# Optimization experiments

Hardware: AMD Instinct MI355X
Metric: run time of the kernel (lower is better)

Reference implementation:

```python
import jax, jax.numpy as jnp
import numpy as np

B, T, D, H, W = 4, 2048, 256, 512, 32
EPS = 1e-5


def _xavier(key, fan_in, fan_out):
    # torch xavier_uniform on weight [out, in]; stored here as [in, out]
    limit = float(np.sqrt(6.0 / (fan_in + fan_out)))
    return jax.random.uniform(key, (fan_in, fan_out), jnp.float32, -limit, limit)


def _bias(key, fan_in, fan_out):
    # torch Linear default bias init: U(-1/sqrt(fan_in), 1/sqrt(fan_in))
    limit = float(1.0 / np.sqrt(fan_in))
    return jax.random.uniform(key, (fan_out,), jnp.float32, -limit, limit)


def setup_inputs() -> dict:
    key = jax.random.key(0)
    ks = jax.random.split(key, 16)
    inp = {
        "feature": jax.random.normal(ks[0], (B, T, D), jnp.float32),
        "gamma": jnp.ones((D,), jnp.float32),
        "beta": jnp.zeros((D,), jnp.float32),
        "w1": _xavier(ks[1], D, H), "b1": _bias(ks[2], D, H),
        "w2": _xavier(ks[3], H, H), "b2": _bias(ks[4], H, H),
        "w3": _xavier(ks[5], D, H), "b3": _bias(ks[6], H, H),
        "w4": _xavier(ks[7], H, H), "b4": _bias(ks[8], H, H),
        "w5": _xavier(ks[9], D, H), "b5": _bias(ks[10], H, H),
        "w6": _xavier(ks[11], H, H), "b6": _bias(ks[12], H, H),
        "window": W,
    }
    return inp


def reference(feature, gamma, beta, w1, b1, w2, b2, w3, b3, w4, b4, w5, b5, w6, b6, window):
    Bsz, Tlen, Din = feature.shape
    nb = Tlen // window
    x = feature.reshape(Bsz, nb, window, Din)  # [B, nb, W, D] window blocks

    # LayerNorm over last dim
    mu = jnp.mean(x, axis=-1, keepdims=True)
    var = jnp.mean((x - mu) ** 2, axis=-1, keepdims=True)
    n = (x - mu) * jax.lax.rsqrt(var + EPS) * gamma + beta

    Q = jnp.tanh(n @ w1 + b1) @ w2 + b2  # [B, nb, W, H]
    K = jnp.tanh(n @ w3 + b3) @ w4 + b4
    V = jax.nn.relu(n @ w5 + b5) @ w6 + b6

    Hdim = w2.shape[1]
    sqrt_feat = jnp.sqrt(jnp.float32(Hdim))
    sqrt_time = jnp.sqrt(jnp.float32(window))

    # time-axis attention: [B, nb, W, W]
    beta_time = jnp.einsum('bnwh,bnvh->bnwv', Q, K) / sqrt_feat
    # feature-axis attention: [B, nb, H, H]
    beta_feat = jnp.einsum('bnwh,bnwg->bnhg', Q, K) / sqrt_time

    A_time = jax.nn.softmax(beta_time, axis=-1)
    A_feat = jax.nn.softmax(beta_feat, axis=-2)

    feat = jnp.einsum('bnwh,bnhg->bnwg', V, A_feat)   # V @ A_feat
    out = jnp.einsum('bnwv,bnvg->bnwg', A_time, feat)  # A_time @ (V @ A_feat)
    return out.reshape(Bsz, Tlen, Hdim)
```

## Files before the change

### kernel.cpp

```cpp
#include <hip/hip_runtime.h>
#include <hip/hip_bf16.h>

typedef unsigned short u16;
typedef __attribute__((ext_vector_type(8))) unsigned short ushort8;
typedef __attribute__((ext_vector_type(8))) short short8;
typedef __attribute__((ext_vector_type(4))) float f32x4;
typedef __attribute__((ext_vector_type(4))) unsigned uint4_t;

#define DEV __device__ __forceinline__

DEV float b2f(u16 u){ return __uint_as_float(((unsigned)u) << 16); }
DEV unsigned cvtpk(float lo, float hi){
  unsigned r;
  asm("v_cvt_pk_bf16_f32 %0, %1, %2" : "=v"(r) : "v"(lo), "v"(hi));
  return r;
}
DEV u16 f2b(float f){ return (u16)cvtpk(f, f); }
DEV void pl32swap(unsigned& a, unsigned& b){
  asm("v_permlane32_swap_b32 %0, %1" : "+v"(a), "+v"(b));
}
DEV void pl16swap(unsigned& a, unsigned& b){
  asm("v_permlane16_swap_b32 %0, %1" : "+v"(a), "+v"(b));
}
DEV float fexp2(float x){
  float r;
  asm("v_exp_f32 %0, %1" : "=v"(r) : "v"(x));
  return r;
}
DEV float frcp(float x){
  float r;
  asm("v_rcp_f32 %0, %1" : "=v"(r) : "v"(x));
  return r;
}
DEV short8 ld8(const u16* p){ return __builtin_bit_cast(short8, *(const ushort8*)p); }
DEV f32x4 mfma(short8 a, short8 b, f32x4 c){
  return __builtin_amdgcn_mfma_f32_16x16x32_bf16(a, b, c, 0, 0, 0);
}
DEV float fast_tanh(float x){
  float e = fexp2(x * 2.8853900817779268f);
  return 1.f - 2.f * frcp(e + 1.f);
}
DEV unsigned pk2(float lo, float hi){ return cvtpk(lo, hi); }

__global__ __launch_bounds__(256) void prep_k(
    const float* __restrict__ w1, const float* __restrict__ w2,
    const float* __restrict__ w3, const float* __restrict__ w4,
    const float* __restrict__ w5, const float* __restrict__ w6,
    u16* __restrict__ ws,
    const float* __restrict__ xg, const float* __restrict__ gg,
    const float* __restrict__ bgm, u16* __restrict__ ng)
{
  __shared__ u16 tile[64][72];
  const int bid = blockIdx.x;
  if (bid < 384) {
    const int z = bid / 64, rem = bid % 64, by = rem / 8, bx = rem % 8;
    const float* w; u16* wt; int K;
    switch (z) {
      case 0:  w = w1; wt = ws;          K = 256; break;
      case 1:  w = w2; wt = ws + 131072; K = 512; break;
      case 2:  w = w3; wt = ws + 393216; K = 256; break;
      case 3:  w = w4; wt = ws + 524288; K = 512; break;
      case 4:  w = w5; wt = ws + 786432; K = 256; break;
      default: w = w6; wt = ws + 917504; K = 512; break;
    }
    int k0 = by * 64;
    if (k0 >= K) return;
    int n0 = bx * 64;
    int t = threadIdx.x;
    int r = t >> 2, c0 = (t & 3) * 16;
    const float* src = w + (size_t)(k0 + r) * 512 + n0 + c0;
    #pragma unroll
    for (int jj = 0; jj < 4; ++jj) {
      float4 v = *(const float4*)(src + jj * 4);
      unsigned* tp = (unsigned*)&tile[r][c0 + jj*4];
      tp[0] = cvtpk(v.x, v.y);
      tp[1] = cvtpk(v.z, v.w);
    }
    __syncthreads();
    ushort8 o0, o1;
    #pragma unroll
    for (int j = 0; j < 8; ++j) { o0[j] = tile[c0 + j][r]; o1[j] = tile[c0 + 8 + j][r]; }
    u16* dst = wt + (size_t)(n0 + r) * K + k0 + c0;
    *(ushort8*)dst       = o0;
    *(ushort8*)(dst + 8) = o1;
  } else {
    const int lb = bid - 384;
    int row = lb * 8 + (threadIdx.x >> 5);
    int l32 = threadIdx.x & 31;
    const float* xr = xg + (size_t)row*256 + l32*8;
    float xf[8];
    #pragma unroll
    for (int j = 0; j < 8; j += 4) {
      float4 v = *(const float4*)(xr + j);
      xf[j] = v.x; xf[j+1] = v.y; xf[j+2] = v.z; xf[j+3] = v.w;
    }
    float s = 0.f, ss = 0.f;
    #pragma unroll
    for (int j = 0; j < 8; ++j){ s += xf[j]; ss += xf[j]*xf[j]; }
    #pragma unroll
    for (int m = 1; m < 32; m <<= 1){ s += __shfl_xor(s, m); ss += __shfl_xor(ss, m); }
    float mean = s * (1.f/256.f);
    float var  = ss * (1.f/256.f) - mean*mean;
    float rs   = rsqrtf(var + 1e-5f);
    float r8[8];
    #pragma unroll
    for (int j = 0; j < 8; j += 4) {
      float4 gv = *(const float4*)(gg  + l32*8 + j);
      float4 bv = *(const float4*)(bgm + l32*8 + j);
      r8[j]   = (xf[j]   - mean)*rs*gv.x + bv.x;
      r8[j+1] = (xf[j+1] - mean)*rs*gv.y + bv.y;
      r8[j+2] = (xf[j+2] - mean)*rs*gv.z + bv.z;
      r8[j+3] = (xf[j+3] - mean)*rs*gv.w + bv.w;
    }
    uint4_t o;
    o[0] = cvtpk(r8[0], r8[1]); o[1] = cvtpk(r8[2], r8[3]);
    o[2] = cvtpk(r8[4], r8[5]); o[3] = cvtpk(r8[6], r8[7]);
    *(uint4_t*)(ng + (size_t)row*256 + l32*8) = o;
  }
}

template<int NS, int ACT>
__global__ __launch_bounds__(512, 4) void gemm_tile(
    const u16* __restrict__ Abase, size_t a_zstride,
    const u16* __restrict__ wst, int w_off0,
    const float* __restrict__ bz0, const float* __restrict__ bz1, const float* __restrict__ bz2,
    u16* __restrict__ Cbase)
{
  constexpr int KA = NS * 32;
  __shared__ __align__(16) u16 sm[20480];
  u16* smA = sm;
  u16* smB = sm + 10240;
  const int z = blockIdx.z;
  const u16* A = Abase + (size_t)z * a_zstride;
  const u16* W = wst + w_off0 + z * 393216;
  const float* bias = (z == 0) ? bz0 : ((z == 1) ? bz1 : bz2);
  u16* C = Cbase + (size_t)z * 4194304;
  const int M0 = blockIdx.x * 128, N0 = blockIdx.y * 128;
  const int tid = threadIdx.x;
  const int wv = tid >> 6, ln = tid & 63, q = ln >> 4, r16 = ln & 15;
  const int m0w = (wv >> 2) * 64, n0w = (wv & 3) * 32;
  const f32x4 Z = {0.f, 0.f, 0.f, 0.f};

  const int srow = tid >> 2, scq = (tid & 3) * 8;
  const u16* gA = A + (size_t)(M0 + srow) * KA + scq;
  const u16* gB = W + (size_t)(N0 + srow) * KA + scq;
  u16* dA = smA + srow * 40 + scq;
  u16* dB = smB + srow * 40 + scq;

  ushort8 rA[2], rB[2];
  rA[0] = *(const ushort8*)gA;
  rB[0] = *(const ushort8*)gB;
  *(ushort8*)dA = rA[0];
  *(ushort8*)dB = rB[0];
  if (NS > 1) { rA[1] = *(const ushort8*)(gA + 32); rB[1] = *(const ushort8*)(gB + 32); }
  __syncthreads();

  f32x4 acc[4][2];
  #pragma unroll
  for (int mf = 0; mf < 4; ++mf){ acc[mf][0] = Z; acc[mf][1] = Z; }

  #pragma unroll
  for (int kk = 0; kk < NS; ++kk) {
    const int cur = kk & 1;
    const u16* bufA = smA + cur * 5120;
    const u16* bufB = smB + cur * 5120;
    short8 aF[4], bF[2];
    #pragma unroll
    for (int mf = 0; mf < 4; ++mf) aF[mf] = ld8(bufA + (m0w + mf*16 + r16)*40 + q*8);
    #pragma unroll
    for (int nf = 0; nf < 2; ++nf) bF[nf] = ld8(bufB + (n0w + nf*16 + r16)*40 + q*8);
    #pragma unroll
    for (int mf = 0; mf < 4; ++mf)
      #pragma unroll
      for (int nf = 0; nf < 2; ++nf)
        acc[mf][nf] = mfma(aF[mf], bF[nf], acc[mf][nf]);
    if (kk + 1 < NS) {
      *(ushort8*)(dA + (cur ^ 1) * 5120) = rA[(kk + 1) & 1];
      *(ushort8*)(dB + (cur ^ 1) * 5120) = rB[(kk + 1) & 1];
    }
    if (kk + 2 < NS) {
      rA[kk & 1] = *(const ushort8*)(gA + (kk + 2) * 32);
      rB[kk & 1] = *(const ushort8*)(gB + (kk + 2) * 32);
    }
    __syncthreads();
  }

  u16* ct = sm;
  #pragma unroll
  for (int nf = 0; nf < 2; ++nf) {
    int colL = n0w + nf*16 + r16;
    float bs = bias[N0 + colL];
    #pragma unroll
    for (int mf = 0; mf < 4; ++mf)
      #pragma unroll
      for (int i = 0; i < 4; ++i) {
        int row = m0w + mf*16 + q*4 + i;
        float v = acc[mf][nf][i] + bs;
        if (ACT == 1) v = fmaxf(v, 0.f);
        else if (ACT == 3) v = (z == 2) ? fmaxf(v, 0.f) : fast_tanh(v);
        ct[row*132 + colL] = f2b(v);
      }
  }
  __syncthreads();
  #pragma unroll
  for (int j = 0; j < 4; ++j) {
    int row = (tid >> 4) + j*32;
    int cb2 = (tid & 15) * 8;
    ushort8 vv = *(const ushort8*)(ct + row*132 + cb2);
    *(ushort8*)(C + (size_t)(M0 + row)*512 + N0 + cb2) = vv;
  }
}

#define AV   0
#define AQT  16640
#define AKT  37120
#define ABT  57600
#define AAT  59712
#define ASM_ELS 60992

__global__ __launch_bounds__(1024) void attn_k(
    const u16* __restrict__ QKVg, float* __restrict__ outg)
{
  __shared__ __align__(16) u16 sm[ASM_ELS];
  const int tid = threadIdx.x;
  const int bid = blockIdx.x;
  const int wv = tid >> 6, ln = tid & 63, q = ln >> 4, r16 = ln & 15;
  const f32x4 Z = {0.f, 0.f, 0.f, 0.f};
  const float RS512 = 0.04419417382415922f;
  const float C32L2 = 0.25500526676986233f;
  const float LOG2E = 1.4426950408889634f;
  const u16* Qg = QKVg + (size_t)bid * 16384;
  const u16* Kg = QKVg + 4194304 + (size_t)bid * 16384;
  const u16* Vg = QKVg + 8388608 + (size_t)bid * 16384;

  float* btf = (float*)(sm + ABT);
  if (wv < 4) {
    int mt = wv >> 1, nt = wv & 1;
    f32x4 acc = Z;
    const u16* qb = Qg + (mt*16 + r16)*512;
    const u16* kb = Kg + (nt*16 + r16)*512;
    #pragma unroll
    for (int kk = 0; kk < 16; ++kk)
      acc = mfma(ld8(qb + kk*32 + q*8), ld8(kb + kk*32 + q*8), acc);
    #pragma unroll
    for (int i = 0; i < 4; ++i)
      btf[(mt*16 + q*4 + i)*33 + nt*16 + r16] = acc[i] * RS512;
  } else if (wv < 12) {
    int t1 = tid - 256;
    int rp = t1 & 15;
    int cb = (t1 >> 4) * 16;
    const u16* s0 = Qg + (2*rp)*512 + cb;
    const u16* s1 = s0 + 512;
    ushort8 a0 = *(const ushort8*)s0, a1 = *(const ushort8*)(s0 + 8);
    ushort8 c0v = *(const ushort8*)s1, c1v = *(const ushort8*)(s1 + 8);
    unsigned* qt32 = (unsigned*)(sm + AQT);
    #pragma unroll
    for (int j = 0; j < 8; ++j) {
      qt32[(cb + j)*20 + rp]     = (unsigned)a0[j] | ((unsigned)c0v[j] << 16);
      qt32[(cb + 8 + j)*20 + rp] = (unsigned)a1[j] | ((unsigned)c1v[j] << 16);
    }
  } else {
    int t2 = tid - 768;
    int vrow = t2 >> 3, seg = (t2 & 7) * 64;
    const u16* src = Vg + vrow*512 + seg;
    #pragma unroll
    for (int jj = 0; jj < 8; ++jj)
      *(ushort8*)(sm + AV + vrow*520 + seg + jj*8) = *(const ushort8*)(src + jj*8);
  }
  __syncthreads();

  if (tid < 512) {
    int row = tid >> 4, v2 = tid & 15;
    float v0 = btf[row*33 + v2], v1 = btf[row*33 + v2 + 16];
    float m = fmaxf(v0, v1);
    #pragma unroll
    for (int msk = 1; msk < 16; msk <<= 1) m = fmaxf(m, __shfl_xor(m, msk));
    float e0 = fexp2((v0 - m) * LOG2E), e1 = fexp2((v1 - m) * LOG2E);
    float sum = e0 + e1;
    #pragma unroll
    for (int msk = 1; msk < 16; msk <<= 1) sum += __shfl_xor(sum, msk);
    float inv = frcp(sum);
    sm[AAT + row*40 + v2]      = f2b(e0 * inv);
    sm[AAT + row*40 + v2 + 16] = f2b(e1 * inv);
  } else {
    int t1 = tid - 512;
    int rp = t1 & 15;
    int cb = (t1 >> 4) * 16;
    const u16* s0 = Kg + (2*rp)*512 + cb;
    const u16* s1 = s0 + 512;
    ushort8 a0 = *(const ushort8*)s0, a1 = *(const ushort8*)(s0 + 8);
    ushort8 c0v = *(const ushort8*)s1, c1v = *(const ushort8*)(s1 + 8);
    unsigned* kt32 = (unsigned*)(sm + AKT);
    #pragma unroll
    for (int j = 0; j < 8; ++j) {
      kt32[(cb + j)*20 + rp]     = (unsigned)a0[j] | ((unsigned)c0v[j] << 16);
      kt32[(cb + 8 + j)*20 + rp] = (unsigned)a1[j] | ((unsigned)c1v[j] << 16);
    }
  }
  __syncthreads();

  {
    const int g0 = wv * 32;
    f32x4 facc[2][2];
    facc[0][0]=Z; facc[0][1]=Z; facc[1][0]=Z; facc[1][1]=Z;
    float csum[2] = {0.f, 0.f};
    short8 bK[2];
    #pragma unroll
    for (int gt = 0; gt < 2; ++gt)
      bK[gt] = ld8(sm + AKT + (size_t)(g0 + gt*16 + r16)*40 + q*8);

    short8 aQn0 = ld8(sm + AQT + (r16)*40 + q*8);
    short8 aQn1 = ld8(sm + AQT + (16 + r16)*40 + q*8);

    #pragma unroll 2
    for (int ht = 0; ht < 16; ++ht) {
      short8 aQ0 = aQn0, aQ1 = aQn1;
      if (ht < 15) {
        aQn0 = ld8(sm + AQT + ((ht+1)*32 + r16)*40 + q*8);
        aQn1 = ld8(sm + AQT + ((ht+1)*32 + 16 + r16)*40 + q*8);
      }
      f32x4 sv[2][2];
      #pragma unroll
      for (int gt = 0; gt < 2; ++gt) {
        sv[0][gt] = mfma(aQ0, bK[gt], Z);
        sv[1][gt] = mfma(aQ1, bK[gt], Z);
      }
      unsigned D[2][4];
      #pragma unroll
      for (int gt = 0; gt < 2; ++gt) {
        float e[2][4];
        #pragma unroll
        for (int smi = 0; smi < 2; ++smi)
          #pragma unroll
          for (int i = 0; i < 4; ++i) {
            float ev = fexp2(sv[smi][gt][i] * C32L2);
            e[smi][i] = ev;
            csum[gt] += ev;
          }
        #pragma unroll
        for (int k = 0; k < 2; ++k) {
          unsigned w0 = cvtpk(e[0][2*k], e[0][2*k+1]);
          unsigned w1 = cvtpk(e[1][2*k], e[1][2*k+1]);
          pl32swap(w0, w1);
          pl16swap(w0, w1);
          D[gt][k]     = w0;
          D[gt][k + 2] = w1;
        }
      }
      #pragma unroll
      for (int mt = 0; mt < 2; ++mt) {
        short8 aV = ld8(sm + AV + (mt*16 + r16)*520 + ht*32 + q*8);
        #pragma unroll
        for (int gt = 0; gt < 2; ++gt) {
          uint4_t dv = {D[gt][0], D[gt][1], D[gt][2], D[gt][3]};
          short8 bE = __builtin_bit_cast(short8, dv);
          facc[mt][gt] = mfma(aV, bE, facc[mt][gt]);
        }
      }
    }
    float inv[2];
    #pragma unroll
    for (int gt = 0; gt < 2; ++gt) {
      float cs = csum[gt];
      cs += __shfl_xor(cs, 16);
      cs += __shfl_xor(cs, 32);
      inv[gt] = frcp(cs);
    }
    unsigned F[2][4];
    #pragma unroll
    for (int gt = 0; gt < 2; ++gt) {
      float e0n[4], e1n[4];
      #pragma unroll
      for (int i = 0; i < 4; ++i) {
        e0n[i] = facc[0][gt][i] * inv[gt];
        e1n[i] = facc[1][gt][i] * inv[gt];
      }
      #pragma unroll
      for (int k = 0; k < 2; ++k) {
        unsigned w0 = cvtpk(e0n[2*k], e0n[2*k+1]);
        unsigned w1 = cvtpk(e1n[2*k], e1n[2*k+1]);
        pl32swap(w0, w1);
        pl16swap(w0, w1);
        F[gt][k]     = w0;
        F[gt][k + 2] = w1;
      }
    }
    short8 aA0 = ld8(sm + AAT + r16*40 + q*8);
    short8 aA1 = ld8(sm + AAT + (16 + r16)*40 + q*8);
    #pragma unroll
    for (int gt = 0; gt < 2; ++gt) {
      uint4_t fv = {F[gt][0], F[gt][1], F[gt][2], F[gt][3]};
      short8 bF = __builtin_bit_cast(short8, fv);
      f32x4 o0 = mfma(aA0, bF, Z);
      f32x4 o1 = mfma(aA1, bF, Z);
      #pragma unroll
      for (int i = 0; i < 4; ++i) {
        int g = g0 + gt*16 + r16;
        outg[(size_t)(bid*32 + q*4 + i)*512 + g]      = o0[i];
        outg[(size_t)(bid*32 + 16 + q*4 + i)*512 + g] = o1[i];
      }
    }
  }
}


#define OFF_V   0
#define OFF_N   16640
#define OFF_T   25088
#define OFF_Q   41728
#define OFF_K   58368
#define OFF_BT  75008
#define OFF_QT  16640
#define OFF_KT  37120
#define OFF_AT  78080
#define OFF_FT  37120
#define SMEM_ELS 79360

template<int ACT>
DEV void mlp_branch(const u16* __restrict__ nl, u16* __restrict__ tl, u16* __restrict__ ol,
                    const u16* __restrict__ wA, const float* __restrict__ bA,
                    const u16* __restrict__ wB, const float* __restrict__ bB,
                    int wv, int q, int r16)
{
  const f32x4 Z = {0.f, 0.f, 0.f, 0.f};
  const int c0 = wv*32 + r16;
  float biasA0 = bA[c0], biasA1 = bA[c0 + 16];
  float biasB0 = bB[c0], biasB1 = bB[c0 + 16];
  {
    const u16* cp0 = wA + (size_t)c0*256 + q*8;
    const u16* cp1 = cp0 + 16*256;
    const u16* a0p = nl + r16 * 264 + q*8;
    const u16* a1p = nl + (16 + r16) * 264 + q*8;
    f32x4 acc[2][2];
    acc[0][0]=Z; acc[0][1]=Z; acc[1][0]=Z; acc[1][1]=Z;
    #pragma unroll
    for (int kk = 0; kk < 8; ++kk) {
      short8 a0 = ld8(a0p + kk*32);
      short8 a1 = ld8(a1p + kk*32);
      short8 b0 = ld8(cp0 + kk*32);
      short8 b1 = ld8(cp1 + kk*32);
      acc[0][0] = mfma(a0, b0, acc[0][0]);
      acc[1][0] = mfma(a1, b0, acc[1][0]);
      acc[0][1] = mfma(a0, b1, acc[0][1]);
      acc[1][1] = mfma(a1, b1, acc[1][1]);
    }
    #pragma unroll
    for (int gt = 0; gt < 2; ++gt) {
      float bias = gt ? biasA1 : biasA0;
      #pragma unroll
      for (int mt = 0; mt < 2; ++mt)
        #pragma unroll
        for (int i = 0; i < 4; ++i) {
          float v = acc[mt][gt][i] + bias;
          v = (ACT == 0) ? fast_tanh(v) : fmaxf(v, 0.f);
          tl[(mt*16 + q*4 + i)*520 + c0 + gt*16] = f2b(v);
        }
    }
  }
  __syncthreads();
  {
    const u16* cp0 = wB + (size_t)c0*512 + q*8;
    const u16* cp1 = cp0 + 16*512;
    const u16* a0p = tl + r16 * 520 + q*8;
    const u16* a1p = tl + (16 + r16) * 520 + q*8;
    f32x4 acc[2][2];
    acc[0][0]=Z; acc[0][1]=Z; acc[1][0]=Z; acc[1][1]=Z;
    #pragma unroll
    for (int kk = 0; kk < 16; ++kk) {
      short8 a0 = ld8(a0p + kk*32);
      short8 a1 = ld8(a1p + kk*32);
      short8 b0 = ld8(cp0 + kk*32);
      short8 b1 = ld8(cp1 + kk*32);
      acc[0][0] = mfma(a0, b0, acc[0][0]);
      acc[1][0] = mfma(a1, b0, acc[1][0]);
      acc[0][1] = mfma(a0, b1, acc[0][1]);
      acc[1][1] = mfma(a1, b1, acc[1][1]);
    }
    #pragma unroll
    for (int gt = 0; gt < 2; ++gt) {
      float bias = gt ? biasB1 : biasB0;
      #pragma unroll
      for (int mt = 0; mt < 2; ++mt)
        #pragma unroll
        for (int i = 0; i < 4; ++i)
          ol[(mt*16 + q*4 + i)*520 + c0 + gt*16] = f2b(acc[mt][gt][i] + bias);
    }
  }
}

__global__ __launch_bounds__(1024) void fused_main(
    const float* __restrict__ xg, const float* __restrict__ gg, const float* __restrict__ bgm,
    const float* __restrict__ b1, const float* __restrict__ b2, const float* __restrict__ b3,
    const float* __restrict__ b4, const float* __restrict__ b5, const float* __restrict__ b6,
    const u16* __restrict__ wst, float* __restrict__ outg)
{
  __shared__ __align__(16) u16 sm[SMEM_ELS];
  const int tid = threadIdx.x;
  const int bid = blockIdx.x;
  const int wv = tid >> 6, ln = tid & 63, q = ln >> 4, r16 = ln & 15;
  const f32x4 Z = {0.f, 0.f, 0.f, 0.f};
  const float RS512 = 0.04419417382415922f;
  const float C32L2 = 0.25500526676986233f;

  {
    int row = tid >> 5, l32 = tid & 31;
    const float* xr = xg + (size_t)(bid*32 + row)*256 + l32*8;
    float xf[8];
    #pragma unroll
    for (int j = 0; j < 8; j += 4) {
      float4 v = *(const float4*)(xr + j);
      xf[j] = v.x; xf[j+1] = v.y; xf[j+2] = v.z; xf[j+3] = v.w;
    }
    float s = 0.f, ss = 0.f;
    #pragma unroll
    for (int j = 0; j < 8; ++j){ s += xf[j]; ss += xf[j]*xf[j]; }
    #pragma unroll
    for (int m = 1; m < 32; m <<= 1){ s += __shfl_xor(s, m); ss += __shfl_xor(ss, m); }
    float mean = s * (1.f/256.f);
    float var  = ss * (1.f/256.f) - mean*mean;
    float rs   = rsqrtf(var + 1e-5f);
    float gf[8], bf[8];
    #pragma unroll
    for (int j = 0; j < 8; j += 4) {
      float4 gv = *(const float4*)(gg  + l32*8 + j);
      float4 bv = *(const float4*)(bgm + l32*8 + j);
      gf[j] = gv.x; gf[j+1] = gv.y; gf[j+2] = gv.z; gf[j+3] = gv.w;
      bf[j] = bv.x; bf[j+1] = bv.y; bf[j+2] = bv.z; bf[j+3] = bv.w;
    }
    ushort8 o0;
    #pragma unroll
    for (int j = 0; j < 8; ++j)
      o0[j] = f2b((xf[j] - mean)*rs*gf[j] + bf[j]);
    *(ushort8*)(sm + OFF_N + row*264 + l32*8) = o0;
  }
  __syncthreads();

  mlp_branch<0>(sm+OFF_N, sm+OFF_T, sm+OFF_Q, wst,          b1, wst + 131072, b2, wv, q, r16);
  __syncthreads();
  mlp_branch<0>(sm+OFF_N, sm+OFF_T, sm+OFF_K, wst + 393216, b3, wst + 524288, b4, wv, q, r16);
  __syncthreads();
  mlp_branch<1>(sm+OFF_N, sm+OFF_T, sm+OFF_V, wst + 786432, b5, wst + 917504, b6, wv, q, r16);
  __syncthreads();

  float* btf = (float*)(sm + OFF_BT);
  if (wv < 4) {
    int mt = wv >> 1, nt = wv & 1;
    f32x4 acc = Z;
    const u16* qb = sm + OFF_Q + (mt*16 + r16)*520;
    const u16* kb = sm + OFF_K + (nt*16 + r16)*520;
    for (int kk = 0; kk < 16; ++kk)
      acc = mfma(ld8(qb + kk*32 + q*8), ld8(kb + kk*32 + q*8), acc);
    #pragma unroll
    for (int i = 0; i < 4; ++i)
      btf[(mt*16 + q*4 + i)*33 + nt*16 + r16] = acc[i] * RS512;
  } else if (wv < 12) {
    int t1 = tid - 256;
    int row = t1 & 31, cb = (t1 >> 5) * 32;
    const u16* src = sm + OFF_Q + row*520 + cb;
    ushort8 v[4];
    #pragma unroll
    for (int jj = 0; jj < 4; ++jj) v[jj] = *(const ushort8*)(src + jj*8);
    #pragma unroll
    for (int jj = 0; jj < 4; ++jj)
      #pragma unroll
      for (int j = 0; j < 8; ++j)
        sm[OFF_QT + (cb + jj*8 + j)*40 + row] = v[jj][j];
  }
  __syncthreads();

  if (tid < 512) {
    int row = tid >> 4, v2 = tid & 15;
    float v0 = btf[row*33 + v2], v1 = btf[row*33 + v2 + 16];
    float m = fmaxf(v0, v1);
    #pragma unroll
    for (int msk = 1; msk < 16; msk <<= 1) m = fmaxf(m, __shfl_xor(m, msk));
    float e0 = __expf(v0 - m), e1 = __expf(v1 - m);
    float sum = e0 + e1;
    #pragma unroll
    for (int msk = 1; msk < 16; msk <<= 1) sum += __shfl_xor(sum, msk);
    float inv = 1.f / sum;
    sm[OFF_AT + row*40 + v2]      = f2b(e0 * inv);
    sm[OFF_AT + row*40 + v2 + 16] = f2b(e1 * inv);
  } else {
    int t2 = tid - 512;
    int row = t2 & 31, cb = (t2 >> 5) * 32;
    const u16* src = sm + OFF_K + row*520 + cb;
    ushort8 v[4];
    #pragma unroll
    for (int jj = 0; jj < 4; ++jj) v[jj] = *(const ushort8*)(src + jj*8);
    #pragma unroll
    for (int jj = 0; jj < 4; ++jj)
      #pragma unroll
      for (int j = 0; j < 8; ++j)
        sm[OFF_KT + (cb + jj*8 + j)*40 + row] = v[jj][j];
  }
  __syncthreads();

  {
    const int g0 = wv * 32;
    const bool hi32 = (ln >= 32);
    const bool qodd = (q & 1);
    f32x4 facc[2][2];
    facc[0][0]=Z; facc[0][1]=Z; facc[1][0]=Z; facc[1][1]=Z;
    float csum[2] = {0.f, 0.f};
    short8 bK[2];
    #pragma unroll
    for (int gt = 0; gt < 2; ++gt)
      bK[gt] = ld8(sm + OFF_KT + (size_t)(g0 + gt*16 + r16)*40 + q*8);

    #pragma unroll 2
    for (int ht = 0; ht < 16; ++ht) {
      f32x4 sv[2][2];
      #pragma unroll
      for (int smi = 0; smi < 2; ++smi) {
        short8 aQ = ld8(sm + OFF_QT + (ht*32 + smi*16 + r16)*40 + q*8);
        #pragma unroll
        for (int gt = 0; gt < 2; ++gt)
          sv[smi][gt] = mfma(aQ, bK[gt], Z);
      }
      unsigned D[2][4];
      #pragma unroll
      for (int gt = 0; gt < 2; ++gt) {
        float e[2][4];
        #pragma unroll
        for (int smi = 0; smi < 2; ++smi)
          #pragma unroll
          for (int i = 0; i < 4; ++i) {
            float ev = fexp2(sv[smi][gt][i] * C32L2);
            e[smi][i] = ev;
            csum[gt] += ev;
          }
        #pragma unroll
        for (int k = 0; k < 2; ++k) {
          unsigned w0 = pk2(e[0][2*k], e[0][2*k+1]);
          unsigned w1 = pk2(e[1][2*k], e[1][2*k+1]);
          unsigned Pw0 = (unsigned)__shfl_xor((int)w0, 32);
          unsigned Pw1 = (unsigned)__shfl_xor((int)w1, 32);
          unsigned x = hi32 ? Pw1 : w0;
          unsigned y = hi32 ? w1 : Pw0;
          unsigned xs = (unsigned)__shfl_xor((int)x, 16);
          unsigned ys = (unsigned)__shfl_xor((int)y, 16);
          D[gt][k]     = qodd ? ys : x;
          D[gt][k + 2] = qodd ? y  : xs;
        }
      }
      #pragma unroll
      for (int mt = 0; mt < 2; ++mt) {
        short8 aV = ld8(sm + OFF_V + (mt*16 + r16)*520 + ht*32 + q*8);
        #pragma unroll
        for (int gt = 0; gt < 2; ++gt) {
          uint4_t dv = {D[gt][0], D[gt][1], D[gt][2], D[gt][3]};
          short8 bE = __builtin_bit_cast(short8, dv);
          facc[mt][gt] = mfma(aV, bE, facc[mt][gt]);
        }
      }
    }
    float inv[2];
    #pragma unroll
    for (int gt = 0; gt < 2; ++gt) {
      float cs = csum[gt];
      cs += __shfl_xor(cs, 16);
      cs += __shfl_xor(cs, 32);
      inv[gt] = 1.f / cs;
    }
    #pragma unroll
    for (int mt = 0; mt < 2; ++mt)
      #pragma unroll
      for (int gt = 0; gt < 2; ++gt)
        #pragma unroll
        for (int i = 0; i < 4; ++i) {
          int w = mt*16 + q*4 + i;
          int g = g0 + gt*16 + r16;
          sm[OFF_FT + g*40 + w] = f2b(facc[mt][gt][i] * inv[gt]);
        }
  }

  {
    const int g0 = wv * 32;
    short8 aA0 = ld8(sm + OFF_AT + r16*40 + q*8);
    short8 aA1 = ld8(sm + OFF_AT + (16 + r16)*40 + q*8);
    #pragma unroll
    for (int gt = 0; gt < 2; ++gt) {
      short8 bF = ld8(sm + OFF_FT + (size_t)(g0 + gt*16 + r16)*40 + q*8);
      f32x4 o0 = mfma(aA0, bF, Z);
      f32x4 o1 = mfma(aA1, bF, Z);
      #pragma unroll
      for (int i = 0; i < 4; ++i) {
        int g = g0 + gt*16 + r16;
        outg[(size_t)(bid*32 + q*4 + i)*512 + g]      = o0[i];
        outg[(size_t)(bid*32 + 16 + q*4 + i)*512 + g] = o1[i];
      }
    }
  }
}


extern "C" void kernel_launch(void* const* d_in, const int* in_sizes, int n_in,
                              void* d_out, int out_size, void* d_ws, size_t ws_size,
                              hipStream_t stream)
{
  const float* x  = (const float*)d_in[0];
  const float* gm = (const float*)d_in[1];
  const float* bt = (const float*)d_in[2];
  const float* w1 = (const float*)d_in[3];
  const float* b1 = (const float*)d_in[4];
  const float* w2 = (const float*)d_in[5];
  const float* b2 = (const float*)d_in[6];
  const float* w3 = (const float*)d_in[7];
  const float* b3 = (const float*)d_in[8];
  const float* w4 = (const float*)d_in[9];
  const float* b4 = (const float*)d_in[10];
  const float* w5 = (const float*)d_in[11];
  const float* b5 = (const float*)d_in[12];
  const float* w6 = (const float*)d_in[13];
  const float* b6 = (const float*)d_in[14];
  u16* ws  = (u16*)d_ws;
  float* out = (float*)d_out;

  const size_t WT_OFF  = 0;
  const size_t N_OFF   = 1179648;
  const size_t T_OFF   = 3276800;
  const size_t QKV_OFF = 15859712;
  const size_t NEED_BYTES = 28442624ULL * 2ULL;

  if (ws_size >= NEED_BYTES) {
    prep_k<<<1408, 256, 0, stream>>>(w1, w2, w3, w4, w5, w6, ws + WT_OFF,
                                     x, gm, bt, ws + N_OFF);
    gemm_tile<8, 3><<<dim3(64, 4, 3), 512, 0, stream>>>(
        ws + N_OFF, 0, ws + WT_OFF, 0, b1, b3, b5, ws + T_OFF);
    gemm_tile<16, 2><<<dim3(64, 4, 3), 512, 0, stream>>>(
        ws + T_OFF, 4194304, ws + WT_OFF, 131072, b2, b4, b6, ws + QKV_OFF);
    attn_k<<<256, 1024, 0, stream>>>(ws + QKV_OFF, out);
  } else {
    prep_k<<<384, 256, 0, stream>>>(w1, w2, w3, w4, w5, w6, ws + WT_OFF,
                                    x, gm, bt, ws + WT_OFF );
    fused_main<<<256, 1024, 0, stream>>>(x, gm, bt, b1, b2, b3, b4, b5, b6, ws + WT_OFF, out);
  }
}
```

Measured before the change: 71.48 us.

## Fuse the two MLP GEMM layers into one kernel keeping the hidden tile in LDS

Replaces the two separate tiled GEMM launches (first layer with activation, then second layer) with a single kernel. Each block computes a 64-row slice of the first-layer output across all 512 hidden columns, keeps the activated bf16 tile in shared memory, and then runs the second GEMM against it. This removes the global write and reread of the intermediate tensor and one kernel launch. In exchange, operands are loaded directly from global memory with no LDS staging or double buffering, output stores are scattered 2-byte writes, and the larger LDS footprint lowers occupancy.

Result: slower. 102.7 us (+43.7%).

```diff
diff --git a/kernel.cpp b/kernel.cpp
--- a/kernel.cpp
+++ b/kernel.cpp
@@ -119,95 +119,96 @@
   }
 }
 
-template<int NS, int ACT>
-__global__ __launch_bounds__(512, 4) void gemm_tile(
-    const u16* __restrict__ Abase, size_t a_zstride,
-    const u16* __restrict__ wst, int w_off0,
-    const float* __restrict__ bz0, const float* __restrict__ bz1, const float* __restrict__ bz2,
-    u16* __restrict__ Cbase)
+#define TSTR 516
+__global__ __launch_bounds__(512, 2) void mlp_k(
+    const u16* __restrict__ ng, const u16* __restrict__ wst,
+    const float* __restrict__ b1, const float* __restrict__ b3, const float* __restrict__ b5,
+    const float* __restrict__ b2, const float* __restrict__ b4, const float* __restrict__ b6,
+    u16* __restrict__ QKVg)
 {
-  constexpr int KA = NS * 32;
-  __shared__ __align__(16) u16 sm[20480];
-  u16* smA = sm;
-  u16* smB = sm + 10240;
-  const int z = blockIdx.z;
-  const u16* A = Abase + (size_t)z * a_zstride;
-  const u16* W = wst + w_off0 + z * 393216;
-  const float* bias = (z == 0) ? bz0 : ((z == 1) ? bz1 : bz2);
-  u16* C = Cbase + (size_t)z * 4194304;
-  const int M0 = blockIdx.x * 128, N0 = blockIdx.y * 128;
+  __shared__ __align__(16) u16 tl[64 * TSTR];
+  const int M0 = blockIdx.x * 64;
+  const int z  = blockIdx.y;
+  const u16* W1 = wst + (size_t)z * 393216;
+  const u16* W2 = wst + 131072 + (size_t)z * 393216;
+  const float* bA = (z == 0) ? b1 : ((z == 1) ? b3 : b5);
+  const float* bB = (z == 0) ? b2 : ((z == 1) ? b4 : b6);
+  u16* C = QKVg + (size_t)z * 4194304;
   const int tid = threadIdx.x;
   const int wv = tid >> 6, ln = tid & 63, q = ln >> 4, r16 = ln & 15;
-  const int m0w = (wv >> 2) * 64, n0w = (wv & 3) * 32;
   const f32x4 Z = {0.f, 0.f, 0.f, 0.f};
-
-  const int srow = tid >> 2, scq = (tid & 3) * 8;
-  const u16* gA = A + (size_t)(M0 + srow) * KA + scq;
-  const u16* gB = W + (size_t)(N0 + srow) * KA + scq;
-  u16* dA = smA + srow * 40 + scq;
-  u16* dB = smB + srow * 40 + scq;
-
-  ushort8 rA[2], rB[2];
-  rA[0] = *(const ushort8*)gA;
-  rB[0] = *(const ushort8*)gB;
-  *(ushort8*)dA = rA[0];
-  *(ushort8*)dB = rB[0];
-  if (NS > 1) { rA[1] = *(const ushort8*)(gA + 32); rB[1] = *(const ushort8*)(gB + 32); }
-  __syncthreads();
-
-  f32x4 acc[4][2];
-  #pragma unroll
-  for (int mf = 0; mf < 4; ++mf){ acc[mf][0] = Z; acc[mf][1] = Z; }
-
-  #pragma unroll
-  for (int kk = 0; kk < NS; ++kk) {
-    const int cur = kk & 1;
-    const u16* bufA = smA + cur * 5120;
-    const u16* bufB = smB + cur * 5120;
-    short8 aF[4], bF[2];
-    #pragma unroll
-    for (int mf = 0; mf < 4; ++mf) aF[mf] = ld8(bufA + (m0w + mf*16 + r16)*40 + q*8);
-    #pragma unroll
-    for (int nf = 0; nf < 2; ++nf) bF[nf] = ld8(bufB + (n0w + nf*16 + r16)*40 + q*8);
+  const u16* nA = ng + (size_t)M0 * 256;
+
+  {
+    f32x4 acc[4][4];
     #pragma unroll
     for (int mf = 0; mf < 4; ++mf)
       #pragma unroll
-      for (int nf = 0; nf < 2; ++nf)
-        acc[mf][nf] = mfma(aF[mf], bF[nf], acc[mf][nf]);
-    if (kk + 1 < NS) {
-      *(ushort8*)(dA + (cur ^ 1) * 5120) = rA[(kk + 1) & 1];
-      *(ushort8*)(dB + (cur ^ 1) * 5120) = rB[(kk + 1) & 1];
-    }
-    if (kk + 2 < NS) {
-      rA[kk & 1] = *(const ushort8*)(gA + (kk + 2) * 32);
-      rB[kk & 1] = *(const ushort8*)(gB + (kk + 2) * 32);
-    }
-    __syncthreads();
-  }
-
-  u16* ct = sm;
-  #pragma unroll
-  for (int nf = 0; nf < 2; ++nf) {
-    int colL = n0w + nf*16 + r16;
-    float bs = bias[N0 + colL];
+      for (int nf = 0; nf < 4; ++nf) acc[mf][nf] = Z;
+    #pragma unroll
+    for (int kk = 0; kk < 8; ++kk) {
+      short8 aF[4], bF[4];
+      #pragma unroll
+      for (int mf = 0; mf < 4; ++mf)
+        aF[mf] = ld8(nA + (size_t)(mf*16 + r16)*256 + kk*32 + q*8);
+      #pragma unroll
+      for (int nf = 0; nf < 4; ++nf)
+        bF[nf] = ld8(W1 + (size_t)(wv*64 + nf*16 + r16)*256 + kk*32 + q*8);
+      #pragma unroll
+      for (int mf = 0; mf < 4; ++mf)
+        #pragma unroll
+        for (int nf = 0; nf < 4; ++nf)
+          acc[mf][nf] = mfma(aF[mf], bF[nf], acc[mf][nf]);
+    }
+    #pragma unroll
+    for (int nf = 0; nf < 4; ++nf) {
+      int col = wv*64 + nf*16 + r16;
+      float bs = bA[col];
+      #pragma unroll
+      for (int mf = 0; mf < 4; ++mf)
+        #pragma unroll
+        for (int i = 0; i < 4; ++i) {
+          float v = acc[mf][nf][i] + bs;
+          v = (z == 2) ? fmaxf(v, 0.f) : fast_tanh(v);
+          tl[(mf*16 + q*4 + i)*TSTR + col] = f2b(v);
+        }
+    }
+  }
+  __syncthreads();
+
+  {
+    f32x4 acc[4][4];
     #pragma unroll
     for (int mf = 0; mf < 4; ++mf)
       #pragma unroll
-      for (int i = 0; i < 4; ++i) {
-        int row = m0w + mf*16 + q*4 + i;
-        float v = acc[mf][nf][i] + bs;
-        if (ACT == 1) v = fmaxf(v, 0.f);
-        else if (ACT == 3) v = (z == 2) ? fmaxf(v, 0.f) : fast_tanh(v);
-        ct[row*132 + colL] = f2b(v);
-      }
-  }
-  __syncthreads();
-  #pragma unroll
-  for (int j = 0; j < 4; ++j) {
-    int row = (tid >> 4) + j*32;
-    int cb2 = (tid & 15) * 8;
-    ushort8 vv = *(const ushort8*)(ct + row*132 + cb2);
-    *(ushort8*)(C + (size_t)(M0 + row)*512 + N0 + cb2) = vv;
+      for (int nf = 0; nf < 4; ++nf) acc[mf][nf] = Z;
+    #pragma unroll
+    for (int kk = 0; kk < 16; ++kk) {
+      short8 aF[4], bF[4];
+      #pragma unroll
+      for (int mf = 0; mf < 4; ++mf)
+        aF[mf] = ld8(tl + (mf*16 + r16)*TSTR + kk*32 + q*8);
+      #pragma unroll
+      for (int nf = 0; nf < 4; ++nf)
+        bF[nf] = ld8(W2 + (size_t)(wv*64 + nf*16 + r16)*512 + kk*32 + q*8);
+      #pragma unroll
+      for (int mf = 0; mf < 4; ++mf)
+        #pragma unroll
+        for (int nf = 0; nf < 4; ++nf)
+          acc[mf][nf] = mfma(aF[mf], bF[nf], acc[mf][nf]);
+    }
+    #pragma unroll
+    for (int nf = 0; nf < 4; ++nf) {
+      int col = wv*64 + nf*16 + r16;
+      float bs = bB[col];
+      #pragma unroll
+      for (int mf = 0; mf < 4; ++mf)
+        #pragma unroll
+        for (int i = 0; i < 4; ++i) {
+          int row = mf*16 + q*4 + i;
+          C[(size_t)(M0 + row)*512 + col] = f2b(acc[mf][nf][i] + bs);
+        }
+    }
   }
 }
 
@@ -719,17 +720,14 @@
 
   const size_t WT_OFF  = 0;
   const size_t N_OFF   = 1179648;
-  const size_t T_OFF   = 3276800;
   const size_t QKV_OFF = 15859712;
   const size_t NEED_BYTES = 28442624ULL * 2ULL;
 
   if (ws_size >= NEED_BYTES) {
     prep_k<<<1408, 256, 0, stream>>>(w1, w2, w3, w4, w5, w6, ws + WT_OFF,
                                      x, gm, bt, ws + N_OFF);
-    gemm_tile<8, 3><<<dim3(64, 4, 3), 512, 0, stream>>>(
-        ws + N_OFF, 0, ws + WT_OFF, 0, b1, b3, b5, ws + T_OFF);
-    gemm_tile<16, 2><<<dim3(64, 4, 3), 512, 0, stream>>>(
-        ws + T_OFF, 4194304, ws + WT_OFF, 131072, b2, b4, b6, ws + QKV_OFF);
+    mlp_k<<<dim3(128, 3), 512, 0, stream>>>(
+        ws + N_OFF, ws + WT_OFF, b1, b3, b5, b2, b4, b6, ws + QKV_OFF);
     attn_k<<<256, 1024, 0, stream>>>(ws + QKV_OFF, out);
   } else {
     prep_k<<<384, 256, 0, stream>>>(w1, w2, w3, w4, w5, w6, ws + WT_OFF,
```

## Read V directly from global in attention loop, shrink LDS padding

Applied to the files above, without the earlier changes.

The attention kernel no longer stages the V block in shared memory. Each wave loads its V fragments straight from global memory inside the head loop. The Q/K transposed tiles use a tighter row stride (36 instead of 40 elements), read with split 8-byte loads, and the Q prefetch is replaced by in-loop loads. Together these cut LDS from about 122KB to about 80KB per block, and launch bounds request higher occupancy. The cost is repeated global/L2 reads of V across the 16 waves, plus narrower LDS loads.

Measured after the change: 102.6 us. 43.5% more time.

```diff
diff --git a/kernel.cpp b/kernel.cpp
--- a/kernel.cpp
+++ b/kernel.cpp
@@ -3,6 +3,7 @@
 
 typedef unsigned short u16;
 typedef __attribute__((ext_vector_type(8))) unsigned short ushort8;
+typedef __attribute__((ext_vector_type(4))) unsigned short ushort4_t;
 typedef __attribute__((ext_vector_type(8))) short short8;
 typedef __attribute__((ext_vector_type(4))) float f32x4;
 typedef __attribute__((ext_vector_type(4))) unsigned uint4_t;
@@ -33,6 +34,14 @@
   return r;
 }
 DEV short8 ld8(const u16* p){ return __builtin_bit_cast(short8, *(const ushort8*)p); }
+DEV short8 ld8s(const u16* p){
+  ushort4_t a = *(const ushort4_t*)p;
+  ushort4_t b = *(const ushort4_t*)(p + 4);
+  ushort8 v;
+  #pragma unroll
+  for (int j = 0; j < 4; ++j){ v[j] = a[j]; v[j+4] = b[j]; }
+  return __builtin_bit_cast(short8, v);
+}
 DEV f32x4 mfma(short8 a, short8 b, f32x4 c){
   return __builtin_amdgcn_mfma_f32_16x16x32_bf16(a, b, c, 0, 0, 0);
 }
@@ -211,17 +220,16 @@
   }
 }
 
-#define AV   0
-#define AQT  16640
-#define AKT  37120
-#define ABT  57600
-#define AAT  59712
-#define ASM_ELS 60992
-
-__global__ __launch_bounds__(1024) void attn_k(
+#define AQT3  0
+#define AKT3  18432
+#define ABT3  36864
+#define AAT3  38976
+#define ASM3_ELS 40256
+
+__global__ __launch_bounds__(1024, 8) void attn_k(
     const u16* __restrict__ QKVg, float* __restrict__ outg)
 {
-  __shared__ __align__(16) u16 sm[ASM_ELS];
+  __shared__ __align__(16) u16 sm[ASM3_ELS];
   const int tid = threadIdx.x;
   const int bid = blockIdx.x;
   const int wv = tid >> 6, ln = tid & 63, q = ln >> 4, r16 = ln & 15;
@@ -233,7 +241,7 @@
   const u16* Kg = QKVg + 4194304 + (size_t)bid * 16384;
   const u16* Vg = QKVg + 8388608 + (size_t)bid * 16384;
 
-  float* btf = (float*)(sm + ABT);
+  float* btf = (float*)(sm + ABT3);
   if (wv < 4) {
     int mt = wv >> 1, nt = wv & 1;
     f32x4 acc = Z;
@@ -253,19 +261,12 @@
     const u16* s1 = s0 + 512;
     ushort8 a0 = *(const ushort8*)s0, a1 = *(const ushort8*)(s0 + 8);
     ushort8 c0v = *(const ushort8*)s1, c1v = *(const ushort8*)(s1 + 8);
-    unsigned* qt32 = (unsigned*)(sm + AQT);
+    unsigned* qt32 = (unsigned*)(sm + AQT3);
     #pragma unroll
     for (int j = 0; j < 8; ++j) {
-      qt32[(cb + j)*20 + rp]     = (unsigned)a0[j] | ((unsigned)c0v[j] << 16);
-      qt32[(cb + 8 + j)*20 + rp] = (unsigned)a1[j] | ((unsigned)c1v[j] << 16);
-    }
-  } else {
-    int t2 = tid - 768;
-    int vrow = t2 >> 3, seg = (t2 & 7) * 64;
-    const u16* src = Vg + vrow*512 + seg;
-    #pragma unroll
-    for (int jj = 0; jj < 8; ++jj)
-      *(ushort8*)(sm + AV + vrow*520 + seg + jj*8) = *(const ushort8*)(src + jj*8);
+      qt32[(cb + j)*18 + rp]     = (unsigned)a0[j] | ((unsigned)c0v[j] << 16);
+      qt32[(cb + 8 + j)*18 + rp] = (unsigned)a1[j] | ((unsigned)c1v[j] << 16);
+    }
   }
   __syncthreads();
 
@@ -280,8 +281,8 @@
     #pragma unroll
     for (int msk = 1; msk < 16; msk <<= 1) sum += __shfl_xor(sum, msk);
     float inv = frcp(sum);
-    sm[AAT + row*40 + v2]      = f2b(e0 * inv);
-    sm[AAT + row*40 + v2 + 16] = f2b(e1 * inv);
+    sm[AAT3 + row*40 + v2]      = f2b(e0 * inv);
+    sm[AAT3 + row*40 + v2 + 16] = f2b(e1 * inv);
   } else {
     int t1 = tid - 512;
     int rp = t1 & 15;
@@ -290,11 +291,11 @@
     const u16* s1 = s0 + 512;
     ushort8 a0 = *(const ushort8*)s0, a1 = *(const ushort8*)(s0 + 8);
     ushort8 c0v = *(const ushort8*)s1, c1v = *(const ushort8*)(s1 + 8);
-    unsigned* kt32 = (unsigned*)(sm + AKT);
+    unsigned* kt32 = (unsigned*)(sm + AKT3);
     #pragma unroll
     for (int j = 0; j < 8; ++j) {
-      kt32[(cb + j)*20 + rp]     = (unsigned)a0[j] | ((unsigned)c0v[j] << 16);
-      kt32[(cb + 8 + j)*20 + rp] = (unsigned)a1[j] | ((unsigned)c1v[j] << 16);
+      kt32[(cb + j)*18 + rp]     = (unsigned)a0[j] | ((unsigned)c0v[j] << 16);
+      kt32[(cb + 8 + j)*18 + rp] = (unsigned)a1[j] | ((unsigned)c1v[j] << 16);
     }
   }
   __syncthreads();
@@ -307,23 +308,21 @@
     short8 bK[2];
     #pragma unroll
     for (int gt = 0; gt < 2; ++gt)
-      bK[gt] = ld8(sm + AKT + (size_t)(g0 + gt*16 + r16)*40 + q*8);
-
-    short8 aQn0 = ld8(sm + AQT + (r16)*40 + q*8);
-    short8 aQn1 = ld8(sm + AQT + (16 + r16)*40 + q*8);
+      bK[gt] = ld8s(sm + AKT3 + (g0 + gt*16 + r16)*36 + q*8);
 
     #pragma unroll 2
     for (int ht = 0; ht < 16; ++ht) {
-      short8 aQ0 = aQn0, aQ1 = aQn1;
-      if (ht < 15) {
-        aQn0 = ld8(sm + AQT + ((ht+1)*32 + r16)*40 + q*8);
-        aQn1 = ld8(sm + AQT + ((ht+1)*32 + 16 + r16)*40 + q*8);
-      }
+      short8 aV[2];
+      #pragma unroll
+      for (int mt = 0; mt < 2; ++mt)
+        aV[mt] = ld8(Vg + (mt*16 + r16)*512 + ht*32 + q*8);
       f32x4 sv[2][2];
       #pragma unroll
-      for (int gt = 0; gt < 2; ++gt) {
-        sv[0][gt] = mfma(aQ0, bK[gt], Z);
-        sv[1][gt] = mfma(aQ1, bK[gt], Z);
+      for (int smi = 0; smi < 2; ++smi) {
+        short8 aQ = ld8s(sm + AQT3 + (ht*32 + smi*16 + r16)*36 + q*8);
+        #pragma unroll
+        for (int gt = 0; gt < 2; ++gt)
+          sv[smi][gt] = mfma(aQ, bK[gt], Z);
       }
       unsigned D[2][4];
       #pragma unroll
@@ -348,15 +347,13 @@
         }
       }
       #pragma unroll
-      for (int mt = 0; mt < 2; ++mt) {
-        short8 aV = ld8(sm + AV + (mt*16 + r16)*520 + ht*32 + q*8);
+      for (int mt = 0; mt < 2; ++mt)
         #pragma unroll
         for (int gt = 0; gt < 2; ++gt) {
           uint4_t dv = {D[gt][0], D[gt][1], D[gt][2], D[gt][3]};
           short8 bE = __builtin_bit_cast(short8, dv);
-          facc[mt][gt] = mfma(aV, bE, facc[mt][gt]);
+          facc[mt][gt] = mfma(aV[mt], bE, facc[mt][gt]);
         }
-      }
     }
     float inv[2];
     #pragma unroll
@@ -385,8 +382,8 @@
         F[gt][k + 2] = w1;
       }
     }
-    short8 aA0 = ld8(sm + AAT + r16*40 + q*8);
-    short8 aA1 = ld8(sm + AAT + (16 + r16)*40 + q*8);
+    short8 aA0 = ld8(sm + AAT3 + r16*40 + q*8);
+    short8 aA1 = ld8(sm + AAT3 + (16 + r16)*40 + q*8);
     #pragma unroll
     for (int gt = 0; gt < 2; ++gt) {
       uint4_t fv = {F[gt][0], F[gt][1], F[gt][2], F[gt][3]};
```
